# Kernel tuning notes

Measured on AMD Instinct MI355X. Metric: run time of the kernel, lower is better.

## Reference

```python
import jax, jax.numpy as jnp
import numpy as np
import math

NUM_HEADS = 4
NUM_GROUPS = 16
EPS = 1e-5


def setup_inputs() -> dict:
    key = jax.random.key(0)
    ks = jax.random.split(key, 4)
    C = 256
    x = jax.random.normal(ks[0], (1, C, 16, 16, 16), dtype=jnp.float32)
    gn_gamma = jnp.ones((C,), dtype=jnp.float32)
    gn_beta = jnp.zeros((C,), dtype=jnp.float32)
    # conv3d 1x1 kernels == plain matrices [out_ch, in_ch]
    w_qkv = jax.random.normal(ks[1], (3 * C, C), dtype=jnp.float32) * (1.0 / math.sqrt(C))
    w_proj = jax.random.normal(ks[2], (C, C), dtype=jnp.float32) * (1.0 / math.sqrt(C))
    b_proj = jnp.zeros((C,), dtype=jnp.float32)
    return {"x": x, "gn_gamma": gn_gamma, "gn_beta": gn_beta,
            "w_qkv": w_qkv, "w_proj": w_proj, "b_proj": b_proj}


def reference(x, gn_gamma, gn_beta, w_qkv, w_proj, b_proj):
    B, C, H, W, D = x.shape
    N = H * W * D
    heads = NUM_HEADS
    d = C // heads

    xf = x.reshape(B, C, N)  # [B, C, N]

    # GroupNorm(16, C) with affine params
    xg = xf.reshape(B, NUM_GROUPS, C // NUM_GROUPS, N)
    mu = jnp.mean(xg, axis=(2, 3), keepdims=True)
    var = jnp.var(xg, axis=(2, 3), keepdims=True)
    xn = ((xg - mu) * jax.lax.rsqrt(var + EPS)).reshape(B, C, N)
    xn = xn * gn_gamma[None, :, None] + gn_beta[None, :, None]

    # 1x1 conv QKV: [B, 3C, N]
    qkv = jnp.einsum('oc,bcn->bon', w_qkv, xn)
    # torch: qkv.reshape(B*heads, 3d, N).chunk(3, dim=1)
    qkv = qkv.reshape(B * heads, 3 * d, N)
    q, k, v = qkv[:, :d], qkv[:, d:2 * d], qkv[:, 2 * d:]

    scale = 1.0 / math.sqrt(math.sqrt(d))
    attn = jnp.einsum('bct,bcs->bts', q * scale, k * scale)  # [B*heads, N, N]
    attn = jax.nn.softmax(attn, axis=-1)
    h = jnp.einsum('bts,bcs->bct', attn, v)  # [B*heads, d, N]

    h = h.reshape(B, C, N)
    out = jnp.einsum('oc,bcn->bon', w_proj, h) + b_proj[None, :, None]
    return (out + xf).reshape(B, C, H, W, D)
```

## Files before the change

### kernel.cpp

```cpp
#include <hip/hip_runtime.h>
#include <math.h>

#define N_TOK 4096
#define C_CH  256
#define SPLITS 4

typedef short bf16x8 __attribute__((ext_vector_type(8)));
typedef float f32x4  __attribute__((ext_vector_type(4)));
typedef unsigned short u16;

__device__ __forceinline__ u16 f2bf(float f) {
    union { float f; unsigned u; } v; v.f = f;
    unsigned r = v.u + 0x7FFF + ((v.u >> 16) & 1);
    return (u16)(r >> 16);
}
__device__ __forceinline__ float bf2f(u16 b) {
    union { unsigned u; float f; } v; v.u = ((unsigned)b) << 16;
    return v.f;
}
__device__ __forceinline__ unsigned packtr(float a, float b) {
    union { float f; unsigned u; } ua, ub; ua.f = a; ub.f = b;
    return __builtin_amdgcn_perm(ub.u, ua.u, 0x07060302u);
}

__global__ __launch_bounds__(256) void wcvt(const float* __restrict__ wqkv,
                                            const float* __restrict__ wproj,
                                            u16* __restrict__ wq, u16* __restrict__ wp) {
    int i = blockIdx.x * 256 + threadIdx.x;
    if (i < 196608) {
        int row = i >> 8;
        float s = ((row % 192) < 64) ? 0.125f : 1.0f;
        wq[i] = f2bf(wqkv[i] * s);
    } else {
        wp[i - 196608] = f2bf(wproj[i - 196608]);
    }
}

__global__ __launch_bounds__(256) void gn_part(const float* __restrict__ x,
                                               float2* __restrict__ part) {
    const int b = blockIdx.x, tid = threadIdx.x;
    const int lane = tid & 63, wave = tid >> 6;
    const float4* xp = (const float4*)x + b * 1024;
    float s = 0.f, ss = 0.f;
#pragma unroll
    for (int k = 0; k < 4; ++k) {
        float4 v = xp[tid + k * 256];
        s  += v.x + v.y + v.z + v.w;
        ss += v.x * v.x + v.y * v.y + v.z * v.z + v.w * v.w;
    }
#pragma unroll
    for (int off = 1; off < 64; off <<= 1) {
        s  += __shfl_xor(s, off, 64);
        ss += __shfl_xor(ss, off, 64);
    }
    __shared__ float rs[4], rss[4];
    if (lane == 0) { rs[wave] = s; rss[wave] = ss; }
    __syncthreads();
    if (tid == 0) part[b] = make_float2(rs[0]+rs[1]+rs[2]+rs[3], rss[0]+rss[1]+rss[2]+rss[3]);
}

__global__ void gn_fin(const float2* __restrict__ part, float* __restrict__ stats) {
    int g = threadIdx.x;
    if (g < 16) {
        float s = 0.f, ss = 0.f;
        for (int j = 0; j < 16; ++j) { float2 p = part[g * 16 + j]; s += p.x; ss += p.y; }
        float mu = s / 65536.f;
        float var = ss / 65536.f - mu * mu;
        stats[g * 2] = mu;
        stats[g * 2 + 1] = rsqrtf(var + 1e-5f);
    }
}

__global__ __launch_bounds__(256) void norm_t(const float* __restrict__ x,
                                              const float* __restrict__ stats,
                                              const float* __restrict__ gamma,
                                              const float* __restrict__ beta,
                                              u16* __restrict__ xt) {
    const int tb = blockIdx.x * 64, cb = blockIdx.y * 64;
    const int tid = threadIdx.x;
    __shared__ float T[64][65];
#pragma unroll
    for (int it = 0; it < 16; ++it) {
        int idx = tid + it * 256;
        int c = idx >> 6, t = idx & 63;
        int cg = cb + c;
        float mu = stats[(cg >> 4) * 2], rstd = stats[(cg >> 4) * 2 + 1];
        T[c][t] = (x[cg * N_TOK + tb + t] - mu) * rstd * gamma[cg] + beta[cg];
    }
    __syncthreads();
#pragma unroll
    for (int it = 0; it < 16; ++it) {
        int idx = tid + it * 256;
        int t = idx >> 6, c = idx & 63;
        xt[(tb + t) * C_CH + cb + c] = f2bf(T[c][t]);
    }
}

__global__ __launch_bounds__(256) void qkv_gemm(const u16* __restrict__ wq,
                                                const u16* __restrict__ xt,
                                                u16* __restrict__ QT,
                                                u16* __restrict__ KTm,
                                                u16* __restrict__ Vc) {
    const int nb = blockIdx.x * 64;
    const int mo = blockIdx.y * 64 + (threadIdx.x >> 6) * 16;
    const int lane = threadIdx.x & 63;
    const int quad = lane >> 4, low = lane & 15;

    f32x4 acc[4] = {f32x4{0,0,0,0}, f32x4{0,0,0,0}, f32x4{0,0,0,0}, f32x4{0,0,0,0}};
#pragma unroll
    for (int kc = 0; kc < 8; ++kc) {
        bf16x8 af = *(const bf16x8*)(wq + (mo + low) * 256 + kc * 32 + quad * 8);
#pragma unroll
        for (int nt = 0; nt < 4; ++nt) {
            bf16x8 bf_ = *(const bf16x8*)(xt + (nb + nt * 16 + low) * 256 + kc * 32 + quad * 8);
            acc[nt] = __builtin_amdgcn_mfma_f32_16x16x32_bf16(af, bf_, acc[nt], 0, 0, 0);
        }
    }
#pragma unroll
    for (int r = 0; r < 4; ++r) {
        int o = mo + quad * 4 + r;
        int head = o / 192, rem = o % 192, c = rem & 63;
#pragma unroll
        for (int nt = 0; nt < 4; ++nt) {
            int tok = nb + nt * 16 + low;
            u16 v = f2bf(acc[nt][r]);
            if (rem < 64)       QT [(head * N_TOK + tok) * 64 + c] = v;
            else if (rem < 128) KTm[(head * N_TOK + tok) * 64 + c] = v;
            else                Vc [(head * 64 + c) * N_TOK + tok] = v;
        }
    }
}

__global__ __launch_bounds__(256, 2) void attn_kernel(const u16* __restrict__ QT,
                                                      const u16* __restrict__ KTm,
                                                      const u16* __restrict__ Vc,
                                                      u16* __restrict__ Op,
                                                      float* __restrict__ Lp) {
    const int head = blockIdx.y, split = blockIdx.z;
    const int qb   = blockIdx.x * 128;
    const int tid  = threadIdx.x;
    const int wave = tid >> 6, lane = tid & 63;
    const int quad = lane >> 4, low = lane & 15;

    const u16* Qh = QT  + head * N_TOK * 64;
    const u16* Kh = KTm + head * N_TOK * 64 + split * 1024 * 64;
    const u16* Vh = Vc  + head * 64 * N_TOK + split * 1024;

    __shared__ u16 Ks[64 * 64];
    __shared__ u16 Vs[64 * 64];
    __shared__ u16 Ps[4 * 32 * 64];
    u16* Pw = Ps + wave * 2048;

    bf16x8 ones;
#pragma unroll
    for (int i = 0; i < 8; ++i) ones[i] = (short)0x3F80;

    bf16x8 bq[2][2];
#pragma unroll
    for (int tn = 0; tn < 2; ++tn)
#pragma unroll
        for (int kh = 0; kh < 2; ++kh)
            bq[tn][kh] = *(const bf16x8*)(Qh + (qb + wave * 32 + tn * 16 + low) * 64 + kh * 32 + quad * 8);

    f32x4 oa[2][4], lC[2];
#pragma unroll
    for (int mt = 0; mt < 2; ++mt) {
        lC[mt] = f32x4{0,0,0,0};
#pragma unroll
        for (int cn = 0; cn < 4; ++cn) oa[mt][cn] = f32x4{0,0,0,0};
    }

    const int sA = tid >> 3, gA = tid & 7;
    const int swA = ((gA ^ (sA & 7)) * 8);
    const int swB = ((gA ^ ((sA + 32) & 7)) * 8);
    uint4 pk0 = *(const uint4*)(Kh + sA * 64 + gA * 8);
    uint4 pk1 = *(const uint4*)(Kh + (sA + 32) * 64 + gA * 8);
    uint4 pv0 = *(const uint4*)(Vh + sA * N_TOK + gA * 8);
    uint4 pv1 = *(const uint4*)(Vh + (sA + 32) * N_TOK + gA * 8);

    const int low7 = low & 7;

    for (int kt = 0; kt < 16; ++kt) {
        __syncthreads();
        *(uint4*)(Ks + sA * 64 + swA) = pk0;
        *(uint4*)(Ks + (sA + 32) * 64 + swB) = pk1;
        *(uint4*)(Vs + sA * 64 + swA) = pv0;
        *(uint4*)(Vs + (sA + 32) * 64 + swB) = pv1;
        if (kt < 15) {
            int sb2 = (kt + 1) * 64;
            pk0 = *(const uint4*)(Kh + (sb2 + sA) * 64 + gA * 8);
            pk1 = *(const uint4*)(Kh + (sb2 + sA + 32) * 64 + gA * 8);
            pv0 = *(const uint4*)(Vh + sA * N_TOK + sb2 + gA * 8);
            pv1 = *(const uint4*)(Vh + (sA + 32) * N_TOK + sb2 + gA * 8);
        }
        __syncthreads();

        f32x4 sa[4][2];
#pragma unroll
        for (int sm = 0; sm < 4; ++sm)
#pragma unroll
            for (int tn = 0; tn < 2; ++tn) sa[sm][tn] = f32x4{0,0,0,0};
#pragma unroll
        for (int kh = 0; kh < 2; ++kh)
#pragma unroll
            for (int sm = 0; sm < 4; ++sm) {
                bf16x8 ak = *(const bf16x8*)(Ks + (sm * 16 + low) * 64 + (((quad + 4 * kh) ^ low7) * 8));
#pragma unroll
                for (int tn = 0; tn < 2; ++tn)
                    sa[sm][tn] = __builtin_amdgcn_mfma_f32_16x16x32_bf16(ak, bq[tn][kh], sa[sm][tn], 0, 0, 0);
            }

#pragma unroll
        for (int sm = 0; sm < 4; ++sm)
#pragma unroll
            for (int tn = 0; tn < 2; ++tn) {
                float p0 = __expf(sa[sm][tn][0]);
                float p1 = __expf(sa[sm][tn][1]);
                float p2 = __expf(sa[sm][tn][2]);
                float p3 = __expf(sa[sm][tn][3]);
                uint2 pk; pk.x = packtr(p0, p1); pk.y = packtr(p2, p3);
                int t = tn * 16 + low;
                int sw = ((sm * 2 + (quad >> 1)) ^ low7);
                *(uint2*)(Pw + t * 64 + sw * 8 + (quad & 1) * 4) = pk;
            }
        asm volatile("s_waitcnt lgkmcnt(0)" ::: "memory");

#pragma unroll
        for (int kh = 0; kh < 2; ++kh) {
            bf16x8 ap0 = *(const bf16x8*)(Pw + (low) * 64      + (((quad + 4 * kh) ^ low7) * 8));
            bf16x8 ap1 = *(const bf16x8*)(Pw + (16 + low) * 64 + (((quad + 4 * kh) ^ low7) * 8));
            lC[0] = __builtin_amdgcn_mfma_f32_16x16x32_bf16(ap0, ones, lC[0], 0, 0, 0);
            lC[1] = __builtin_amdgcn_mfma_f32_16x16x32_bf16(ap1, ones, lC[1], 0, 0, 0);
#pragma unroll
            for (int cn = 0; cn < 4; ++cn) {
                bf16x8 bv = *(const bf16x8*)(Vs + (cn * 16 + low) * 64 + (((quad + 4 * kh) ^ low7) * 8));
                oa[0][cn] = __builtin_amdgcn_mfma_f32_16x16x32_bf16(ap0, bv, oa[0][cn], 0, 0, 0);
                oa[1][cn] = __builtin_amdgcn_mfma_f32_16x16x32_bf16(ap1, bv, oa[1][cn], 0, 0, 0);
            }
        }
    }

    const int sh = (split * 4 + head) * N_TOK;
#pragma unroll
    for (int mt = 0; mt < 2; ++mt)
#pragma unroll
        for (int r = 0; r < 4; ++r) {
            int t = qb + wave * 32 + mt * 16 + quad * 4 + r;
            if (low == 0) Lp[sh + t] = lC[mt][r];
#pragma unroll
            for (int cn = 0; cn < 4; ++cn)
                Op[(sh + t) * 64 + cn * 16 + low] = f2bf(oa[mt][cn][r]);
        }
}

__global__ __launch_bounds__(256) void combine(const u16* __restrict__ Op,
                                               const float* __restrict__ Lp,
                                               u16* __restrict__ hT) {
    int row = blockIdx.x * 4 + (threadIdx.x >> 6);
    int head = row >> 12, t = row & 4095, c = threadIdx.x & 63;
    float o = 0.f, l = 0.f;
#pragma unroll
    for (int sp = 0; sp < SPLITS; ++sp) {
        int b = (sp * 4 + head) * N_TOK + t;
        o += bf2f(Op[b * 64 + c]);
        l += Lp[b];
    }
    hT[t * C_CH + head * 64 + c] = f2bf(o / l);
}

__global__ __launch_bounds__(256) void proj_gemm(const u16* __restrict__ wp,
                                                 const u16* __restrict__ hT,
                                                 const float* __restrict__ bias,
                                                 const float* __restrict__ xres,
                                                 float* __restrict__ out) {
    const int nb = blockIdx.x * 32;
    const int mo = blockIdx.y * 64 + (threadIdx.x >> 6) * 16;
    const int lane = threadIdx.x & 63;
    const int quad = lane >> 4, low = lane & 15;

    f32x4 acc[2] = {f32x4{0,0,0,0}, f32x4{0,0,0,0}};
#pragma unroll
    for (int kc = 0; kc < 8; ++kc) {
        bf16x8 af = *(const bf16x8*)(wp + (mo + low) * 256 + kc * 32 + quad * 8);
#pragma unroll
        for (int nt = 0; nt < 2; ++nt) {
            bf16x8 bf_ = *(const bf16x8*)(hT + (nb + nt * 16 + low) * 256 + kc * 32 + quad * 8);
            acc[nt] = __builtin_amdgcn_mfma_f32_16x16x32_bf16(af, bf_, acc[nt], 0, 0, 0);
        }
    }
#pragma unroll
    for (int r = 0; r < 4; ++r) {
        int o = mo + quad * 4 + r;
        float bv = bias[o];
#pragma unroll
        for (int nt = 0; nt < 2; ++nt) {
            int tok = nb + nt * 16 + low;
            out[o * N_TOK + tok] = acc[nt][r] + bv + xres[o * N_TOK + tok];
        }
    }
}

extern "C" void kernel_launch(void* const* d_in, const int* in_sizes, int n_in,
                              void* d_out, int out_size, void* d_ws, size_t ws_size,
                              hipStream_t stream) {
    const float* x      = (const float*)d_in[0];
    const float* gamma  = (const float*)d_in[1];
    const float* beta   = (const float*)d_in[2];
    const float* w_qkv  = (const float*)d_in[3];
    const float* w_proj = (const float*)d_in[4];
    const float* b_proj = (const float*)d_in[5];
    float* out = (float*)d_out;

    char* base = (char*)d_ws;
    u16*    Op    = (u16*)base;
    u16*    xt    = (u16*)base;
    float*  Lp    = (float*)(base + 8388608);
    float*  stats = (float*)(base + 8650752);
    float2* part  = (float2*)(base + 8654848);
    u16*    wq    = (u16*)(base + 8658944);
    u16*    wp    = (u16*)(base + 9052160);
    u16*    QT    = (u16*)(base + 9183232);
    u16*    hT    = QT;
    u16*    KTm   = (u16*)(base + 11280384);
    u16*    Vc    = (u16*)(base + 13377536);

    wcvt      <<<1024, 256, 0, stream>>>(w_qkv, w_proj, wq, wp);
    gn_part   <<<256, 256, 0, stream>>>(x, part);
    gn_fin    <<<1, 64, 0, stream>>>(part, stats);
    norm_t    <<<dim3(64, 4),  256, 0, stream>>>(x, stats, gamma, beta, xt);
    qkv_gemm  <<<dim3(64, 12), 256, 0, stream>>>(wq, xt, QT, KTm, Vc);
    attn_kernel<<<dim3(32, 4, SPLITS), 256, 0, stream>>>(QT, KTm, Vc, Op, Lp);
    combine   <<<4096, 256, 0, stream>>>(Op, Lp, hT);
    proj_gemm <<<dim3(128, 4), 256, 0, stream>>>(wp, hT, b_proj, x, out);
}
```

Before: 130.2 us.

## Fuse prep kernels, fold GN finalize into norm, merge split-combine into proj GEMM

Merges the weight conversion and GroupNorm partial sums into one launch, moves the GN stats finalization into norm_t, and folds the split-K attention combine into proj_gemm through a shared-memory hT tile with a wider 64-token block. This cuts the launch count from 8 to 5 and drops the hT round trip through global memory. In exchange, every norm_t block redundantly recomputes the group stats, and each proj_gemm block re-reads Op and Lp for all 4 output-channel blocks.

```diff
diff --git a/kernel.cpp b/kernel.cpp
--- a/kernel.cpp
+++ b/kernel.cpp
@@ -23,69 +23,67 @@
     return __builtin_amdgcn_perm(ub.u, ua.u, 0x07060302u);
 }
 
-__global__ __launch_bounds__(256) void wcvt(const float* __restrict__ wqkv,
+__global__ __launch_bounds__(256) void prep(const float* __restrict__ wqkv,
                                             const float* __restrict__ wproj,
-                                            u16* __restrict__ wq, u16* __restrict__ wp) {
-    int i = blockIdx.x * 256 + threadIdx.x;
-    if (i < 196608) {
-        int row = i >> 8;
-        float s = ((row % 192) < 64) ? 0.125f : 1.0f;
-        wq[i] = f2bf(wqkv[i] * s);
+                                            const float* __restrict__ x,
+                                            u16* __restrict__ wq, u16* __restrict__ wp,
+                                            float2* __restrict__ part) {
+    __shared__ float rs[4], rss[4];
+    if (blockIdx.x < 1024) {
+        int i = blockIdx.x * 256 + threadIdx.x;
+        if (i < 196608) {
+            int row = i >> 8;
+            float s = ((row % 192) < 64) ? 0.125f : 1.0f;
+            wq[i] = f2bf(wqkv[i] * s);
+        } else {
+            wp[i - 196608] = f2bf(wproj[i - 196608]);
+        }
     } else {
-        wp[i - 196608] = f2bf(wproj[i - 196608]);
-    }
-}
-
-__global__ __launch_bounds__(256) void gn_part(const float* __restrict__ x,
-                                               float2* __restrict__ part) {
-    const int b = blockIdx.x, tid = threadIdx.x;
-    const int lane = tid & 63, wave = tid >> 6;
-    const float4* xp = (const float4*)x + b * 1024;
-    float s = 0.f, ss = 0.f;
-#pragma unroll
-    for (int k = 0; k < 4; ++k) {
-        float4 v = xp[tid + k * 256];
-        s  += v.x + v.y + v.z + v.w;
-        ss += v.x * v.x + v.y * v.y + v.z * v.z + v.w * v.w;
-    }
-#pragma unroll
-    for (int off = 1; off < 64; off <<= 1) {
-        s  += __shfl_xor(s, off, 64);
-        ss += __shfl_xor(ss, off, 64);
-    }
-    __shared__ float rs[4], rss[4];
-    if (lane == 0) { rs[wave] = s; rss[wave] = ss; }
-    __syncthreads();
-    if (tid == 0) part[b] = make_float2(rs[0]+rs[1]+rs[2]+rs[3], rss[0]+rss[1]+rss[2]+rss[3]);
-}
-
-__global__ void gn_fin(const float2* __restrict__ part, float* __restrict__ stats) {
-    int g = threadIdx.x;
-    if (g < 16) {
+        const int b = blockIdx.x - 1024, tid = threadIdx.x;
+        const int lane = tid & 63, wave = tid >> 6;
+        const float4* xp = (const float4*)x + b * 1024;
         float s = 0.f, ss = 0.f;
-        for (int j = 0; j < 16; ++j) { float2 p = part[g * 16 + j]; s += p.x; ss += p.y; }
-        float mu = s / 65536.f;
-        float var = ss / 65536.f - mu * mu;
-        stats[g * 2] = mu;
-        stats[g * 2 + 1] = rsqrtf(var + 1e-5f);
+#pragma unroll
+        for (int k = 0; k < 4; ++k) {
+            float4 v = xp[tid + k * 256];
+            s  += v.x + v.y + v.z + v.w;
+            ss += v.x * v.x + v.y * v.y + v.z * v.z + v.w * v.w;
+        }
+#pragma unroll
+        for (int off = 1; off < 64; off <<= 1) {
+            s  += __shfl_xor(s, off, 64);
+            ss += __shfl_xor(ss, off, 64);
+        }
+        if (lane == 0) { rs[wave] = s; rss[wave] = ss; }
+        __syncthreads();
+        if (tid == 0) part[b] = make_float2(rs[0]+rs[1]+rs[2]+rs[3], rss[0]+rss[1]+rss[2]+rss[3]);
     }
 }
 
 __global__ __launch_bounds__(256) void norm_t(const float* __restrict__ x,
-                                              const float* __restrict__ stats,
+                                              const float2* __restrict__ part,
                                               const float* __restrict__ gamma,
                                               const float* __restrict__ beta,
                                               u16* __restrict__ xt) {
     const int tb = blockIdx.x * 64, cb = blockIdx.y * 64;
     const int tid = threadIdx.x;
     __shared__ float T[64][65];
+    __shared__ float smu[16], srstd[16];
+    if (tid < 16) {
+        float s = 0.f, ss = 0.f;
+#pragma unroll
+        for (int j = 0; j < 16; ++j) { float2 p = part[tid * 16 + j]; s += p.x; ss += p.y; }
+        float mu = s / 65536.f;
+        float var = ss / 65536.f - mu * mu;
+        smu[tid] = mu; srstd[tid] = rsqrtf(var + 1e-5f);
+    }
+    __syncthreads();
 #pragma unroll
     for (int it = 0; it < 16; ++it) {
         int idx = tid + it * 256;
         int c = idx >> 6, t = idx & 63;
         int cg = cb + c;
-        float mu = stats[(cg >> 4) * 2], rstd = stats[(cg >> 4) * 2 + 1];
-        T[c][t] = (x[cg * N_TOK + tb + t] - mu) * rstd * gamma[cg] + beta[cg];
+        T[c][t] = (x[cg * N_TOK + tb + t] - smu[cg >> 4]) * srstd[cg >> 4] * gamma[cg] + beta[cg];
     }
     __syncthreads();
 #pragma unroll
@@ -253,38 +251,51 @@
         }
 }
 
-__global__ __launch_bounds__(256) void combine(const u16* __restrict__ Op,
-                                               const float* __restrict__ Lp,
-                                               u16* __restrict__ hT) {
-    int row = blockIdx.x * 4 + (threadIdx.x >> 6);
-    int head = row >> 12, t = row & 4095, c = threadIdx.x & 63;
-    float o = 0.f, l = 0.f;
-#pragma unroll
-    for (int sp = 0; sp < SPLITS; ++sp) {
-        int b = (sp * 4 + head) * N_TOK + t;
-        o += bf2f(Op[b * 64 + c]);
-        l += Lp[b];
-    }
-    hT[t * C_CH + head * 64 + c] = f2bf(o / l);
-}
-
 __global__ __launch_bounds__(256) void proj_gemm(const u16* __restrict__ wp,
-                                                 const u16* __restrict__ hT,
+                                                 const u16* __restrict__ Op,
+                                                 const float* __restrict__ Lp,
                                                  const float* __restrict__ bias,
                                                  const float* __restrict__ xres,
                                                  float* __restrict__ out) {
-    const int nb = blockIdx.x * 32;
+    const int nb = blockIdx.x * 64;
     const int mo = blockIdx.y * 64 + (threadIdx.x >> 6) * 16;
     const int lane = threadIdx.x & 63;
     const int quad = lane >> 4, low = lane & 15;
 
-    f32x4 acc[2] = {f32x4{0,0,0,0}, f32x4{0,0,0,0}};
+    __shared__ u16 hT[64 * 264];
+
+#pragma unroll
+    for (int i = 0; i < 8; ++i) {
+        int idx = i * 256 + threadIdx.x;
+        int t = idx >> 5, cc = idx & 31;
+        int head = cc >> 3;
+        int tok = nb + t;
+        float l = 0.f;
+        float o[8] = {0.f,0.f,0.f,0.f,0.f,0.f,0.f,0.f};
+#pragma unroll
+        for (int sp = 0; sp < SPLITS; ++sp) {
+            int b = (sp * 4 + head) * N_TOK + tok;
+            l += Lp[b];
+            uint4 pv = *(const uint4*)(Op + b * 64 + (cc & 7) * 8);
+            const u16* ps = (const u16*)&pv;
+#pragma unroll
+            for (int j = 0; j < 8; ++j) o[j] += bf2f(ps[j]);
+        }
+        float rl = 1.f / l;
+        u16 res[8];
+#pragma unroll
+        for (int j = 0; j < 8; ++j) res[j] = f2bf(o[j] * rl);
+        *(uint4*)(hT + t * 264 + cc * 8) = *(const uint4*)res;
+    }
+    __syncthreads();
+
+    f32x4 acc[4] = {f32x4{0,0,0,0}, f32x4{0,0,0,0}, f32x4{0,0,0,0}, f32x4{0,0,0,0}};
 #pragma unroll
     for (int kc = 0; kc < 8; ++kc) {
         bf16x8 af = *(const bf16x8*)(wp + (mo + low) * 256 + kc * 32 + quad * 8);
 #pragma unroll
-        for (int nt = 0; nt < 2; ++nt) {
-            bf16x8 bf_ = *(const bf16x8*)(hT + (nb + nt * 16 + low) * 256 + kc * 32 + quad * 8);
+        for (int nt = 0; nt < 4; ++nt) {
+            bf16x8 bf_ = *(const bf16x8*)(hT + (nt * 16 + low) * 264 + kc * 32 + quad * 8);
             acc[nt] = __builtin_amdgcn_mfma_f32_16x16x32_bf16(af, bf_, acc[nt], 0, 0, 0);
         }
     }
@@ -293,7 +304,7 @@
         int o = mo + quad * 4 + r;
         float bv = bias[o];
 #pragma unroll
-        for (int nt = 0; nt < 2; ++nt) {
+        for (int nt = 0; nt < 4; ++nt) {
             int tok = nb + nt * 16 + low;
             out[o * N_TOK + tok] = acc[nt][r] + bv + xres[o * N_TOK + tok];
         }
@@ -315,21 +326,16 @@
     u16*    Op    = (u16*)base;
     u16*    xt    = (u16*)base;
     float*  Lp    = (float*)(base + 8388608);
-    float*  stats = (float*)(base + 8650752);
     float2* part  = (float2*)(base + 8654848);
     u16*    wq    = (u16*)(base + 8658944);
     u16*    wp    = (u16*)(base + 9052160);
     u16*    QT    = (u16*)(base + 9183232);
-    u16*    hT    = QT;
     u16*    KTm   = (u16*)(base + 11280384);
     u16*    Vc    = (u16*)(base + 13377536);
 
-    wcvt      <<<1024, 256, 0, stream>>>(w_qkv, w_proj, wq, wp);
-    gn_part   <<<256, 256, 0, stream>>>(x, part);
-    gn_fin    <<<1, 64, 0, stream>>>(part, stats);
-    norm_t    <<<dim3(64, 4),  256, 0, stream>>>(x, stats, gamma, beta, xt);
+    prep      <<<1280, 256, 0, stream>>>(w_qkv, w_proj, x, wq, wp, part);
+    norm_t    <<<dim3(64, 4),  256, 0, stream>>>(x, part, gamma, beta, xt);
     qkv_gemm  <<<dim3(64, 12), 256, 0, stream>>>(wq, xt, QT, KTm, Vc);
     attn_kernel<<<dim3(32, 4, SPLITS), 256, 0, stream>>>(QT, KTm, Vc, Op, Lp);
-    combine   <<<4096, 256, 0, stream>>>(Op, Lp, hT);
-    proj_gemm <<<dim3(128, 4), 256, 0, stream>>>(wp, hT, b_proj, x, out);
-}
+    proj_gemm <<<dim3(64, 4),  256, 0, stream>>>(wp, Op, Lp, b_proj, x, out);
+}
```

Result: faster. 122.8 us (-5.7%).
